# Performance work log

Hardware: AMD Instinct MI355X
Metric: run time of the kernel (lower is better)

## Reference

```python
import jax, jax.numpy as jnp
import numpy as np

KH, KW = 2, 2
GRID_SIZE = 5
SPLINE_ORDER = 3
IN_FEATURES = KH * KW
N_COEF = GRID_SIZE + SPLINE_ORDER  # 8
N_KNOTS = GRID_SIZE + 2 * SPLINE_ORDER + 1  # 12


def b_splines(x, grid, spline_order):
    """x: (N, in), grid: (in, n_knots) -> (N, in, grid_size + spline_order).
    Cox-de-Boor recursion, identical to efficient-kan's b_splines."""
    x_ = x[..., None]  # (N, in, 1)
    bases = ((x_ >= grid[:, :-1]) & (x_ < grid[:, 1:])).astype(x.dtype)
    for k in range(1, spline_order + 1):
        left = (x_ - grid[:, : -(k + 1)]) / (grid[:, k:-1] - grid[:, : -(k + 1)])
        right = (grid[:, k + 1:] - x_) / (grid[:, k + 1:] - grid[:, 1:-k])
        bases = left * bases[..., :-1] + right * bases[..., 1:]
    return bases  # (N, in, N_COEF)


def setup_inputs() -> dict:
    key = jax.random.key(0)
    k1, k2, k3, k4 = jax.random.split(key, 4)
    B, C, H, W = 8, 16, 128, 128
    x = jax.random.normal(k1, (B, C, H, W), dtype=jnp.float32) * 0.5  # mostly inside grid_range
    base_weight = jax.random.normal(k2, (1, IN_FEATURES), dtype=jnp.float32) * 0.5
    spline_weight = jax.random.normal(k3, (1, IN_FEATURES, N_COEF), dtype=jnp.float32) * 0.1
    spline_scaler = 1.0 + jax.random.normal(k4, (1, IN_FEATURES), dtype=jnp.float32) * 0.1
    # uniform extended knot grid over grid_range=[-1, 1], same per input feature (buffer)
    h = 2.0 / GRID_SIZE
    g = np.arange(-SPLINE_ORDER, GRID_SIZE + SPLINE_ORDER + 1, dtype=np.float32) * h - 1.0
    grid = jnp.asarray(np.broadcast_to(g, (IN_FEATURES, N_KNOTS)).copy())
    return {"x": x, "base_weight": base_weight, "spline_weight": spline_weight,
            "spline_scaler": spline_scaler, "grid": grid}


def reference(x, base_weight, spline_weight, spline_scaler, grid):
    B, C, H, W = x.shape
    Ho, Wo = H - KH + 1, W - KW + 1  # stride 1, no padding, no dilation
    # unfold: (B, C, Ho, Wo, KH*KW), window elements in torch Unfold row-major order
    patches = jnp.stack([x[:, :, i:i + Ho, j:j + Wo]
                         for i in range(KH) for j in range(KW)], axis=-1)
    flat = patches.reshape(-1, IN_FEATURES)  # (N, 4)
    # KANLinear: base path (SiLU activation then linear)
    base = jax.nn.silu(flat) @ base_weight.T  # (N, 1)
    # spline path
    bas = b_splines(flat, grid, SPLINE_ORDER)  # (N, 4, 8)
    sw = spline_weight * spline_scaler[..., None]  # scaled_spline_weight (1, 4, 8)
    spline = bas.reshape(flat.shape[0], -1) @ sw.reshape(sw.shape[0], -1).T  # (N, 1)
    out = (base + spline).reshape(B, C, Ho, Wo)
    # multiple_convs_kan_conv2d accumulates the per-channel results into one output channel
    return out.sum(axis=1, keepdims=True)  # (B, 1, Ho, Wo)
```

## Files before the change

### kernel.cpp

```cpp
#include <hip/hip_runtime.h>


#define IN_F 4
#define N_COEF 8
#define N_INT 11
#define TW 32
#define TH 8
#define LW 33
#define LH 9
#define NV (LW * LH)
#define CG 4

__device__ __forceinline__ float silu(float x) {
    return x * __builtin_amdgcn_rcpf(1.0f + __expf(-x));
}

__global__ __launch_bounds__(256) void kan_conv_kernel(
    const float* __restrict__ x,
    const float* __restrict__ base_w,
    const float* __restrict__ spline_w,
    const float* __restrict__ spline_s,
    const float* __restrict__ grid,
    float* __restrict__ out,
    int B, int C, int H, int W)
{
    const int Ho = H - 1, Wo = W - 1;

    __shared__ float4 coef[N_INT][IN_F];
    __shared__ float  sfeat[IN_F][NV];
    __shared__ float  s_misc[6];

    const int tid = threadIdx.x;

    if (tid < N_INT * IN_F) {
        const int t = tid / IN_F;
        const int p = tid % IN_F;
        const float M[4][4] = {
            {1.f/6.f, -3.f/6.f,  3.f/6.f, -1.f/6.f},
            {4.f/6.f,  0.f,     -6.f/6.f,  3.f/6.f},
            {1.f/6.f,  3.f/6.f,  3.f/6.f, -3.f/6.f},
            {0.f,      0.f,      0.f,      1.f/6.f}};
        const float scal = spline_s[p];
        float c0 = 0.f, c1 = 0.f, c2 = 0.f, c3 = 0.f;
        #pragma unroll
        for (int m = 0; m < 4; ++m) {
            const int j = t - 3 + m;
            const float w = (j >= 0 && j < N_COEF)
                              ? spline_w[p * N_COEF + j] * scal : 0.f;
            c0 += M[m][0] * w; c1 += M[m][1] * w;
            c2 += M[m][2] * w; c3 += M[m][3] * w;
        }
        coef[t][p] = make_float4(c0, c1, c2, c3);
    }
    if (tid < IN_F) s_misc[tid] = base_w[tid];
    if (tid == 4)   s_misc[4] = grid[0];
    if (tid == 5)   s_misc[5] = 1.0f / (grid[1] - grid[0]);

    int bid = blockIdx.x;
    const int cg  = bid & 3;  bid >>= 2;
    const int txi = bid & 3;  bid >>= 2;
    const int tyi = bid & 15; bid >>= 4;
    const int b   = bid;
    const int tx0 = txi * TW, ty0 = tyi * TH, c0ch = cg * CG;

    const int lx = tid & (TW - 1);
    const int ly = tid >> 5;
    const int oy = ty0 + ly, ox = tx0 + lx;

    __syncthreads();
    const float bw0 = s_misc[0], bw1 = s_misc[1];
    const float bw2 = s_misc[2], bw3 = s_misc[3];
    const float g0 = s_misc[4], invh = s_misc[5];
    const float bw[4] = {bw0, bw1, bw2, bw3};

    float acc = 0.f;

    #pragma unroll
    for (int g = 0; g < CG; ++g) {
        const int c = c0ch + g;
        const float* __restrict__ xc = x + ((size_t)(b * C + c) * H) * W;

        if (g > 0) __syncthreads();

        #pragma unroll
        for (int v = tid; v < NV; v += 256) {
            const int r  = v / LW;
            const int cc = v - r * LW;
            const int iy = ty0 + r, ix = tx0 + cc;
            const float val = (iy < H && ix < W) ? xc[iy * W + ix] : 0.f;

            const float sil = silu(val);
            const float tf  = (val - g0) * invh;
            const float tfl = floorf(tf);
            const int   ti  = (int)tfl;
            const float u   = tf - tfl;
            const bool  valid = ((unsigned)ti < (unsigned)N_INT);
            const int   tc  = valid ? ti : 0;

            #pragma unroll
            for (int p = 0; p < IN_F; ++p) {
                const float4 cf = coef[tc][p];
                float sp = fmaf(u, cf.w, cf.z);
                sp = fmaf(u, sp, cf.y);
                sp = fmaf(u, sp, cf.x);
                sfeat[p][v] = fmaf(sil, bw[p], valid ? sp : 0.f);
            }
        }
        __syncthreads();

        const int i00 = ly * LW + lx;
        acc += sfeat[0][i00] + sfeat[1][i00 + 1]
             + sfeat[2][i00 + LW] + sfeat[3][i00 + LW + 1];
    }

    if (oy < Ho && ox < Wo)
        atomicAdd(&out[((size_t)b * Ho + oy) * Wo + ox], acc);
}

extern "C" void kernel_launch(void* const* d_in, const int* in_sizes, int n_in,
                              void* d_out, int out_size, void* d_ws, size_t ws_size,
                              hipStream_t stream) {
    const float* x        = (const float*)d_in[0];
    const float* base_w   = (const float*)d_in[1];
    const float* spline_w = (const float*)d_in[2];
    const float* spline_s = (const float*)d_in[3];
    const float* grid     = (const float*)d_in[4];
    float* out = (float*)d_out;

    const int B = 8, C = 16, H = 128, W = 128;

    hipMemsetAsync(out, 0, (size_t)out_size * sizeof(float), stream);

    kan_conv_kernel<<<2048, 256, 0, stream>>>(
        x, base_w, spline_w, spline_s, grid, out, B, C, H, W);
}
```

Baseline: 75.24 us.

## Replace LDS feature staging with register float4 rows and wave shuffles

Each thread now loads two float4 rows covering four output columns and gets its right neighbour through a wave shuffle, so the shared-memory feature buffer and the per-channel barriers go away. Only the spline features a row actually needs are computed (features 0/1 for the top row, 2/3 for the bottom), which cuts redundant spline evaluation. Blocks now cover full 128-wide rows with 2 channels each, giving half as many blocks and four atomics per thread. The cost is that every thread recomputes its own halo row, and the shuffle across the 32-lane group boundary pulls from another row's lane, so the last column relies on that being masked by Wo.

```diff
diff --git a/kernel.cpp b/kernel.cpp
--- a/kernel.cpp
+++ b/kernel.cpp
@@ -4,12 +4,7 @@
 #define IN_F 4
 #define N_COEF 8
 #define N_INT 11
-#define TW 32
-#define TH 8
-#define LW 33
-#define LH 9
-#define NV (LW * LH)
-#define CG 4
+#define CG 2
 
 __device__ __forceinline__ float silu(float x) {
     return x * __builtin_amdgcn_rcpf(1.0f + __expf(-x));
@@ -27,11 +22,9 @@
     const int Ho = H - 1, Wo = W - 1;
 
     __shared__ float4 coef[N_INT][IN_F];
-    __shared__ float  sfeat[IN_F][NV];
     __shared__ float  s_misc[6];
 
     const int tid = threadIdx.x;
-
     if (tid < N_INT * IN_F) {
         const int t = tid / IN_F;
         const int p = tid % IN_F;
@@ -55,66 +48,92 @@
     if (tid < IN_F) s_misc[tid] = base_w[tid];
     if (tid == 4)   s_misc[4] = grid[0];
     if (tid == 5)   s_misc[5] = 1.0f / (grid[1] - grid[0]);
+    __syncthreads();
 
-    int bid = blockIdx.x;
-    const int cg  = bid & 3;  bid >>= 2;
-    const int txi = bid & 3;  bid >>= 2;
-    const int tyi = bid & 15; bid >>= 4;
-    const int b   = bid;
-    const int tx0 = txi * TW, ty0 = tyi * TH, c0ch = cg * CG;
-
-    const int lx = tid & (TW - 1);
-    const int ly = tid >> 5;
-    const int oy = ty0 + ly, ox = tx0 + lx;
-
-    __syncthreads();
     const float bw0 = s_misc[0], bw1 = s_misc[1];
     const float bw2 = s_misc[2], bw3 = s_misc[3];
     const float g0 = s_misc[4], invh = s_misc[5];
-    const float bw[4] = {bw0, bw1, bw2, bw3};
 
-    float acc = 0.f;
+    int bid = blockIdx.x;
+    const int cg  = bid & 7;  bid >>= 3;
+    const int tyi = bid & 15; bid >>= 4;
+    const int b   = bid;
+
+    const int g  = tid & 31;
+    const int r  = tid >> 5;
+    const int oy = tyi * 8 + r;
+    const int ys = (oy < Ho) ? oy : (Ho - 1);
+    const int ox = g * 4;
+
+    float acc0 = 0.f, acc1 = 0.f, acc2 = 0.f, acc3 = 0.f;
 
     #pragma unroll
-    for (int g = 0; g < CG; ++g) {
-        const int c = c0ch + g;
+    for (int cc = 0; cc < CG; ++cc) {
+        const int c = cg * CG + cc;
         const float* __restrict__ xc = x + ((size_t)(b * C + c) * H) * W;
 
-        if (g > 0) __syncthreads();
+        const float4 r0 = *(const float4*)(xc + (size_t)ys * W + ox);
+        const float4 r1 = *(const float4*)(xc + (size_t)(ys + 1) * W + ox);
+        const float a4 = __shfl_down(r0.x, 1);
+        const float b4 = __shfl_down(r1.x, 1);
+
+        const float av[5] = {r0.x, r0.y, r0.z, r0.w, a4};
+        const float bv[5] = {r1.x, r1.y, r1.z, r1.w, b4};
+        float f0[5], f1[5], f2[5], f3[5];
 
         #pragma unroll
-        for (int v = tid; v < NV; v += 256) {
-            const int r  = v / LW;
-            const int cc = v - r * LW;
-            const int iy = ty0 + r, ix = tx0 + cc;
-            const float val = (iy < H && ix < W) ? xc[iy * W + ix] : 0.f;
-
-            const float sil = silu(val);
-            const float tf  = (val - g0) * invh;
-            const float tfl = floorf(tf);
-            const int   ti  = (int)tfl;
-            const float u   = tf - tfl;
-            const bool  valid = ((unsigned)ti < (unsigned)N_INT);
-            const int   tc  = valid ? ti : 0;
-
-            #pragma unroll
-            for (int p = 0; p < IN_F; ++p) {
-                const float4 cf = coef[tc][p];
-                float sp = fmaf(u, cf.w, cf.z);
-                sp = fmaf(u, sp, cf.y);
-                sp = fmaf(u, sp, cf.x);
-                sfeat[p][v] = fmaf(sil, bw[p], valid ? sp : 0.f);
+        for (int k = 0; k < 5; ++k) {
+            {
+                const float v   = av[k];
+                const float sil = silu(v);
+                const float tf  = (v - g0) * invh;
+                const float tfl = floorf(tf);
+                const int   ti  = (int)tfl;
+                const float u   = tf - tfl;
+                const bool  ok  = ((unsigned)ti < (unsigned)N_INT);
+                const int   t   = ok ? ti : 0;
+                const float4 ca = coef[t][0];
+                const float4 cb = coef[t][1];
+                float sa = fmaf(u, ca.w, ca.z);
+                sa = fmaf(u, sa, ca.y); sa = fmaf(u, sa, ca.x);
+                float sb = fmaf(u, cb.w, cb.z);
+                sb = fmaf(u, sb, cb.y); sb = fmaf(u, sb, cb.x);
+                f0[k] = fmaf(sil, bw0, ok ? sa : 0.f);
+                f1[k] = fmaf(sil, bw1, ok ? sb : 0.f);
+            }
+            {
+                const float v   = bv[k];
+                const float sil = silu(v);
+                const float tf  = (v - g0) * invh;
+                const float tfl = floorf(tf);
+                const int   ti  = (int)tfl;
+                const float u   = tf - tfl;
+                const bool  ok  = ((unsigned)ti < (unsigned)N_INT);
+                const int   t   = ok ? ti : 0;
+                const float4 ca = coef[t][2];
+                const float4 cb = coef[t][3];
+                float sa = fmaf(u, ca.w, ca.z);
+                sa = fmaf(u, sa, ca.y); sa = fmaf(u, sa, ca.x);
+                float sb = fmaf(u, cb.w, cb.z);
+                sb = fmaf(u, sb, cb.y); sb = fmaf(u, sb, cb.x);
+                f2[k] = fmaf(sil, bw2, ok ? sa : 0.f);
+                f3[k] = fmaf(sil, bw3, ok ? sb : 0.f);
             }
         }
-        __syncthreads();
 
-        const int i00 = ly * LW + lx;
-        acc += sfeat[0][i00] + sfeat[1][i00 + 1]
-             + sfeat[2][i00 + LW] + sfeat[3][i00 + LW + 1];
+        acc0 += f0[0] + f1[1] + f2[0] + f3[1];
+        acc1 += f0[1] + f1[2] + f2[1] + f3[2];
+        acc2 += f0[2] + f1[3] + f2[2] + f3[3];
+        acc3 += f0[3] + f1[4] + f2[3] + f3[4];
     }
 
-    if (oy < Ho && ox < Wo)
-        atomicAdd(&out[((size_t)b * Ho + oy) * Wo + ox], acc);
+    if (oy < Ho) {
+        float* orow = out + ((size_t)b * Ho + oy) * Wo + ox;
+        atomicAdd(orow + 0, acc0);
+        atomicAdd(orow + 1, acc1);
+        atomicAdd(orow + 2, acc2);
+        if (ox + 3 < Wo) atomicAdd(orow + 3, acc3);
+    }
 }
 
 extern "C" void kernel_launch(void* const* d_in, const int* in_sizes, int n_in,
@@ -131,6 +150,6 @@
 
     hipMemsetAsync(out, 0, (size_t)out_size * sizeof(float), stream);
 
-    kan_conv_kernel<<<2048, 256, 0, stream>>>(
+    kan_conv_kernel<<<1024, 256, 0, stream>>>(
         x, base_w, spline_w, spline_s, grid, out, B, C, H, W);
 }
```

Result: slower. 81.43 us (+8.2%).
